# Optimization experiments

Hardware: AMD Instinct MI355X
Metric: run time of the kernel (lower is better)

Reference implementation:

```python
import jax, jax.numpy as jnp
import numpy as np
import math

B, C, LQ, LK = 8, 128, 2048, 2048

def setup_inputs() -> dict:
    key = jax.random.key(0)
    k1, k2, k3, k4 = jax.random.split(key, 4)
    return {
        "proj_query": jax.random.normal(k1, (B, C, LQ), dtype=jnp.float32),
        "proj_key": jax.random.normal(k2, (B, C, LK), dtype=jnp.float32),
        "proj_val": jax.random.normal(k3, (B, C, LK), dtype=jnp.float32),
        "padding_mask": jax.random.randint(k4, (B, LQ, LK), 0, 2, dtype=jnp.int32),
    }

def reference(proj_query, proj_key, proj_val, padding_mask):
    c = proj_query.shape[1]
    scale = 1.0 / math.sqrt(c)
    # energy: (B, Lq, Lk)
    energy = jnp.einsum('bcq,bck->bqk', proj_query, proj_key) * scale
    mask_f = padding_mask.astype(energy.dtype)
    attention = jax.nn.softmax(energy + jnp.log(mask_f + 1e-9), axis=-1)
    attention = attention * mask_f
    # out: (B, C, Lq)
    out = jnp.einsum('bck,bqk->bcq', proj_val, attention)
    return out, attention
```

## Files before the change

### kernel.cpp

```cpp
#include <hip/hip_runtime.h>
#include <hip/hip_bf16.h>
#include <math.h>

constexpr int NB  = 8;
constexpr int NC  = 128;
constexpr int NLQ = 2048;
constexpr int NLK = 2048;
#define SCALE 0.08838834764831845f

typedef _Float16 h8  __attribute__((ext_vector_type(8)));
typedef _Float16 h4v __attribute__((ext_vector_type(4)));
typedef float    f4  __attribute__((ext_vector_type(4)));
typedef int      i4  __attribute__((ext_vector_type(4)));

__global__ __launch_bounds__(256)
void trans_f32_h16(const float* __restrict__ in, _Float16* __restrict__ out)
{
    __shared__ float tile[32][33];
    const int b  = blockIdx.z;
    const int l0 = blockIdx.x * 32;
    const int c0 = blockIdx.y * 32;
    const int tx = threadIdx.x, ty = threadIdx.y;
    const float* ip = in + ((size_t)(b * NC + c0 + ty)) * NLK + l0 + tx;
    #pragma unroll
    for (int j = 0; j < 4; ++j)
        tile[ty + j * 8][tx] = ip[(size_t)j * 8 * NLK];
    __syncthreads();
    _Float16* op = out + ((size_t)(b * NLK + l0 + ty)) * NC + c0 + tx;
    #pragma unroll
    for (int j = 0; j < 4; ++j)
        op[(size_t)j * 8 * NC] = (_Float16)tile[tx][ty + j * 8];
}

__global__ __launch_bounds__(256)
void cvt_f32_h16(const float* __restrict__ in, _Float16* __restrict__ out, int n4)
{
    const int i = blockIdx.x * blockDim.x + threadIdx.x;
    if (i < n4) {
        const f4 v = *(const f4*)&in[(size_t)i * 4];
        h4v h;
        #pragma unroll
        for (int j = 0; j < 4; ++j) h[j] = (_Float16)v[j];
        *(h4v*)&out[(size_t)i * 4] = h;
    }
}

constexpr int KSTR = 136;
constexpr int PSTR = 72;

__global__ __launch_bounds__(512, 6)
void attn_main(const _Float16* __restrict__ Qt, const _Float16* __restrict__ Kt,
               const _Float16* __restrict__ Vh, const int* __restrict__ Mp,
               float* __restrict__ outP, float* __restrict__ attnP)
{
    __shared__ _Float16 Kl[2][64 * KSTR];
    __shared__ _Float16 pad[2][32 * PSTR];
    __shared__ float sred[32][4];

    const int tid  = threadIdx.x;
    const int w    = tid >> 6;
    const int lane = tid & 63;
    const int lo   = lane & 15;
    const int g    = lane >> 4;
    const int qsub = w & 1;
    const int kh   = w >> 1;

    const int bid   = blockIdx.x;
    const int b     = bid & 7;
    const int q0    = (bid >> 3) * 32;
    const int qbase = q0 + qsub * 16;

    const int krow = tid >> 3, kcs = (tid & 7) * 16;

    h8 aQ[4];
    {
        const _Float16* qr = &Qt[((size_t)(b * NLQ + qbase + lo)) * NC];
        #pragma unroll
        for (int cc = 0; cc < 4; ++cc) aQ[cc] = *(const h8*)&qr[cc * 32 + g * 8];
    }
    const int* mbase = &Mp[((size_t)(b * NLQ + qbase + lo)) * NLK + kh * 16 + g * 4];

    {
        const _Float16* s0 = &Kt[((size_t)(b * NLK + krow)) * NC + kcs];
        const h8 x = *(const h8*)s0, y = *(const h8*)(s0 + 8);
        _Float16* d0 = &Kl[0][krow * KSTR + kcs];
        *(h8*)d0 = x; *(h8*)(d0 + 8) = y;
    }
    i4 mm = *(const i4*)&mbase[0];
    __syncthreads();

    float os = 0.f;
    unsigned long long pk0 = 0ull, pk1 = 0ull;
    for (int t = 0; t < 32; ++t) {
        const int p = t & 1, tn = (t + 1 < 32) ? t + 1 : 31;
        const _Float16* ksp = &Kt[((size_t)(b * NLK + tn * 64 + krow)) * NC + kcs];
        const h8 nk0 = *(const h8*)ksp, nk1 = *(const h8*)(ksp + 8);
        const i4 mmn = *(const i4*)&mbase[(size_t)tn * 64];
        const unsigned int nib = (mm[0] & 1) | ((mm[1] & 1) << 1)
                               | ((mm[2] & 1) << 2) | ((mm[3] & 1) << 3);
        if (t < 16) pk0 |= (unsigned long long)nib << (t * 4);
        else        pk1 |= (unsigned long long)nib << ((t - 16) * 4);
        const _Float16* kr = &Kl[p][(kh * 16 + lo) * KSTR + g * 8];
        f4 d = {0.f, 0.f, 0.f, 0.f};
        d = __builtin_amdgcn_mfma_f32_16x16x32_f16(*(const h8*)&kr[0],  aQ[0], d, 0, 0, 0);
        d = __builtin_amdgcn_mfma_f32_16x16x32_f16(*(const h8*)&kr[32], aQ[1], d, 0, 0, 0);
        d = __builtin_amdgcn_mfma_f32_16x16x32_f16(*(const h8*)&kr[64], aQ[2], d, 0, 0, 0);
        d = __builtin_amdgcn_mfma_f32_16x16x32_f16(*(const h8*)&kr[96], aQ[3], d, 0, 0, 0);
        #pragma unroll
        for (int r = 0; r < 4; ++r)
            os += ((nib >> r) & 1u) ? __expf(d[r] * SCALE) : 0.f;
        _Float16* kd = &Kl[p ^ 1][krow * KSTR + kcs];
        *(h8*)kd = nk0; *(h8*)(kd + 8) = nk1;
        mm = mmn;
        __syncthreads();
    }
    os += __shfl_xor(os, 16);
    os += __shfl_xor(os, 32);
    if (lane < 16) sred[qsub * 16 + lane][kh] = os;
    __syncthreads();
    float inv;
    {
        const float S = sred[qsub * 16 + lo][0] + sred[qsub * 16 + lo][1]
                      + sred[qsub * 16 + lo][2] + sred[qsub * 16 + lo][3];
        inv = S > 0.f ? 1.0f / S : 0.f;
    }

    {
        const _Float16* s0 = &Kt[((size_t)(b * NLK + krow)) * NC + kcs];
        const h8 x = *(const h8*)s0, y = *(const h8*)(s0 + 8);
        _Float16* d0 = &Kl[0][krow * KSTR + kcs];
        *(h8*)d0 = x; *(h8*)(d0 + 8) = y;
    }
    const _Float16* vbase = &Vh[((size_t)(b * NC + w * 16 + lo)) * NLK + g * 8];
    h8 vn0 = *(const h8*)&vbase[0];
    h8 vn1 = *(const h8*)&vbase[32];
    __syncthreads();

    {
        const unsigned int nib = (unsigned int)(pk0 & 0xFull);
        const _Float16* kr = &Kl[0][(kh * 16 + lo) * KSTR + g * 8];
        f4 d = {0.f, 0.f, 0.f, 0.f};
        d = __builtin_amdgcn_mfma_f32_16x16x32_f16(*(const h8*)&kr[0],  aQ[0], d, 0, 0, 0);
        d = __builtin_amdgcn_mfma_f32_16x16x32_f16(*(const h8*)&kr[32], aQ[1], d, 0, 0, 0);
        d = __builtin_amdgcn_mfma_f32_16x16x32_f16(*(const h8*)&kr[64], aQ[2], d, 0, 0, 0);
        d = __builtin_amdgcn_mfma_f32_16x16x32_f16(*(const h8*)&kr[96], aQ[3], d, 0, 0, 0);
        h4v ph;
        #pragma unroll
        for (int r = 0; r < 4; ++r)
            ph[r] = ((nib >> r) & 1u) ? (_Float16)(__expf(d[r] * SCALE) * inv)
                                      : (_Float16)0.f;
        *(h4v*)&pad[0][(qsub * 16 + lo) * PSTR + kh * 16 + g * 4] = ph;
        const _Float16* ksp = &Kt[((size_t)(b * NLK + 64 + krow)) * NC + kcs];
        const h8 nk0 = *(const h8*)ksp, nk1 = *(const h8*)(ksp + 8);
        _Float16* kd = &Kl[1][krow * KSTR + kcs];
        *(h8*)kd = nk0; *(h8*)(kd + 8) = nk1;
    }

    f4 acc0 = {0.f, 0.f, 0.f, 0.f}, acc1 = {0.f, 0.f, 0.f, 0.f};
    const int arow = w * 4 + (lane >> 4);
    const int acol = (lane & 15) * 4;

    for (int t = 0; t < 32; ++t) {
        __syncthreads();
        const int bt = t & 1;
        const h8 v0 = vn0, v1 = vn1;
        if (t < 31) {
            const _Float16* vt = vbase + (size_t)(t + 1) * 64;
            vn0 = *(const h8*)&vt[0];
            vn1 = *(const h8*)&vt[32];
        }
        h8 kn0, kn1;
        if (t < 30) {
            const _Float16* ksp = &Kt[((size_t)(b * NLK + (t + 2) * 64 + krow)) * NC + kcs];
            kn0 = *(const h8*)ksp; kn1 = *(const h8*)(ksp + 8);
        }
        {
            const h4v ph = *(const h4v*)&pad[bt][arow * PSTR + acol];
            f4 av;
            #pragma unroll
            for (int i = 0; i < 4; ++i) av[i] = (float)ph[i];
            *(f4*)&attnP[((size_t)(b * NLQ + q0 + arow)) * NLK + t * 64 + acol] = av;
        }
        {
            const h8 pa00 = *(const h8*)&pad[bt][lo * PSTR + g * 8];
            const h8 pa01 = *(const h8*)&pad[bt][lo * PSTR + 32 + g * 8];
            const h8 pa10 = *(const h8*)&pad[bt][(16 + lo) * PSTR + g * 8];
            const h8 pa11 = *(const h8*)&pad[bt][(16 + lo) * PSTR + 32 + g * 8];
            acc0 = __builtin_amdgcn_mfma_f32_16x16x32_f16(pa00, v0, acc0, 0, 0, 0);
            acc0 = __builtin_amdgcn_mfma_f32_16x16x32_f16(pa01, v1, acc0, 0, 0, 0);
            acc1 = __builtin_amdgcn_mfma_f32_16x16x32_f16(pa10, v0, acc1, 0, 0, 0);
            acc1 = __builtin_amdgcn_mfma_f32_16x16x32_f16(pa11, v1, acc1, 0, 0, 0);
        }
        if (t < 31) {
            const int tt = t + 1;
            const unsigned long long sel = (tt & 16) ? pk1 : pk0;
            const unsigned int nib = (unsigned int)((sel >> ((tt & 15) * 4)) & 0xFull);
            const _Float16* kr = &Kl[tt & 1][(kh * 16 + lo) * KSTR + g * 8];
            f4 d = {0.f, 0.f, 0.f, 0.f};
            d = __builtin_amdgcn_mfma_f32_16x16x32_f16(*(const h8*)&kr[0],  aQ[0], d, 0, 0, 0);
            d = __builtin_amdgcn_mfma_f32_16x16x32_f16(*(const h8*)&kr[32], aQ[1], d, 0, 0, 0);
            d = __builtin_amdgcn_mfma_f32_16x16x32_f16(*(const h8*)&kr[64], aQ[2], d, 0, 0, 0);
            d = __builtin_amdgcn_mfma_f32_16x16x32_f16(*(const h8*)&kr[96], aQ[3], d, 0, 0, 0);
            h4v ph;
            #pragma unroll
            for (int r = 0; r < 4; ++r)
                ph[r] = ((nib >> r) & 1u) ? (_Float16)(__expf(d[r] * SCALE) * inv)
                                          : (_Float16)0.f;
            *(h4v*)&pad[bt ^ 1][(qsub * 16 + lo) * PSTR + kh * 16 + g * 4] = ph;
        }
        if (t < 30) {
            _Float16* kd = &Kl[bt][krow * KSTR + kcs];
            *(h8*)kd = kn0; *(h8*)(kd + 8) = kn1;
        }
    }
    *(f4*)&outP[((size_t)(b * NC + w * 16 + lo)) * NLQ + q0 + g * 4]      = acc0;
    *(f4*)&outP[((size_t)(b * NC + w * 16 + lo)) * NLQ + q0 + 16 + g * 4] = acc1;
}

constexpr int QT_F = 32;
constexpr int SPAD_F = 2056;

__global__ __launch_bounds__(512, 2)
void attn_fallback(const float* __restrict__ Qp, const float* __restrict__ Kp,
                   const float* __restrict__ Vp, const int* __restrict__ Mp,
                   float* __restrict__ outP, float* __restrict__ attnP)
{
    __shared__ _Float16 Sh[QT_F][SPAD_F];
    __shared__ float mred[4][QT_F];
    __shared__ float sred[4][QT_F];

    const int tid  = threadIdx.x;
    const int w    = tid >> 6;
    const int lane = tid & 63;
    const int lo   = lane & 15;
    const int g    = lane >> 4;
    const int qg   = w & 1;
    const int nh   = w >> 1;
    const int b    = blockIdx.y;
    const int q0   = blockIdx.x * QT_F;

    h8 aQ[4];
    {
        const int q = q0 + qg * 16 + lo;
        #pragma unroll
        for (int cc = 0; cc < 4; ++cc) {
            const float* qp = &Qp[((size_t)(b * NC + cc * 32 + g * 8)) * NLQ + q];
            #pragma unroll
            for (int j = 0; j < 8; ++j) aQ[cc][j] = (_Float16)qp[(size_t)j * NLQ];
        }
    }
    float mx[4] = {-INFINITY, -INFINITY, -INFINITY, -INFINITY};
    for (int t = 0; t < 32; ++t) {
        const int n0 = nh * 512 + t * 16;
        f4 d = {0.f, 0.f, 0.f, 0.f};
        #pragma unroll
        for (int cc = 0; cc < 4; ++cc) {
            const float* kp = &Kp[((size_t)(b * NC + cc * 32 + g * 8)) * NLK + n0 + lo];
            h8 bk;
            #pragma unroll
            for (int j = 0; j < 8; ++j) bk[j] = (_Float16)kp[(size_t)j * NLK];
            d = __builtin_amdgcn_mfma_f32_16x16x32_f16(aQ[cc], bk, d, 0, 0, 0);
        }
        const int* mp = &Mp[((size_t)(b * NLQ + q0 + qg * 16 + g * 4)) * NLK + n0 + lo];
        #pragma unroll
        for (int r = 0; r < 4; ++r) {
            float e = d[r] * SCALE;
            const int mv = mp[(size_t)r * NLK];
            e = mv ? e : -INFINITY;
            const _Float16 eh = (_Float16)e;
            mx[r] = fmaxf(mx[r], (float)eh);
            Sh[qg * 16 + g * 4 + r][n0 + lo] = eh;
        }
    }
    #pragma unroll
    for (int off = 1; off < 16; off <<= 1) {
        #pragma unroll
        for (int r = 0; r < 4; ++r) mx[r] = fmaxf(mx[r], __shfl_xor(mx[r], off));
    }
    if (lo == 0) {
        #pragma unroll
        for (int r = 0; r < 4; ++r) mred[nh][qg * 16 + g * 4 + r] = mx[r];
    }
    __syncthreads();
    for (int rr = 0; rr < 16; ++rr) {
        const int row = qg * 16 + rr;
        float m = fmaxf(fmaxf(mred[0][row], mred[1][row]), fmaxf(mred[2][row], mred[3][row]));
        if (m < -1e30f) m = 0.f;
        float s = 0.f;
        #pragma unroll
        for (int it = 0; it < 2; ++it) {
            const int kb = nh * 512 + it * 256 + lane * 4;
            h4v v = *(const h4v*)&Sh[row][kb];
            s += __expf((float)v[0] - m) + __expf((float)v[1] - m)
               + __expf((float)v[2] - m) + __expf((float)v[3] - m);
        }
        #pragma unroll
        for (int off = 1; off < 64; off <<= 1) s += __shfl_xor(s, off);
        if (lane == 0) sred[nh][row] = s;
    }
    __syncthreads();
    for (int rr = 0; rr < 16; ++rr) {
        const int row = qg * 16 + rr;
        float m = fmaxf(fmaxf(mred[0][row], mred[1][row]), fmaxf(mred[2][row], mred[3][row]));
        if (m < -1e30f) m = 0.f;
        const float s = sred[0][row] + sred[1][row] + sred[2][row] + sred[3][row];
        const float inv = s > 0.f ? 1.0f / s : 0.f;
        #pragma unroll
        for (int it = 0; it < 2; ++it) {
            const int kb = nh * 512 + it * 256 + lane * 4;
            h4v v = *(const h4v*)&Sh[row][kb];
            f4 a;
            #pragma unroll
            for (int i = 0; i < 4; ++i) a[i] = __expf((float)v[i] - m) * inv;
            *(f4*)&attnP[((size_t)(b * NLQ + q0 + row)) * NLK + kb] = a;
            h4v hv;
            #pragma unroll
            for (int i = 0; i < 4; ++i) hv[i] = (_Float16)a[i];
            *(h4v*)&Sh[row][kb] = hv;
        }
    }
    __syncthreads();
    f4 acc[2] = {{0.f,0.f,0.f,0.f},{0.f,0.f,0.f,0.f}};
    for (int kt = 0; kt < 64; ++kt) {
        const int k0 = kt * 32;
        const h8 a = *(const h8*)&Sh[qg * 16 + lo][k0 + g * 8];
        #pragma unroll
        for (int ct = 0; ct < 2; ++ct) {
            const int c = nh * 32 + ct * 16 + lo;
            const float* vp = &Vp[((size_t)(b * NC + c)) * NLK + k0 + g * 8];
            const f4 v0 = *(const f4*)vp;
            const f4 v1 = *(const f4*)(vp + 4);
            h8 bv;
            #pragma unroll
            for (int j = 0; j < 4; ++j) { bv[j] = (_Float16)v0[j]; bv[4 + j] = (_Float16)v1[j]; }
            acc[ct] = __builtin_amdgcn_mfma_f32_16x16x32_f16(a, bv, acc[ct], 0, 0, 0);
        }
    }
    #pragma unroll
    for (int ct = 0; ct < 2; ++ct) {
        const int c = nh * 32 + ct * 16 + lo;
        const int q = q0 + qg * 16 + g * 4;
        *(f4*)&outP[((size_t)(b * NC + c)) * NLQ + q] = acc[ct];
    }
}

extern "C" void kernel_launch(void* const* d_in, const int* in_sizes, int n_in,
                              void* d_out, int out_size, void* d_ws, size_t ws_size,
                              hipStream_t stream) {
    const float* Qp = (const float*)d_in[0];
    const float* Kp = (const float*)d_in[1];
    const float* Vp = (const float*)d_in[2];
    const int*   Mp = (const int*)d_in[3];
    float* outP  = (float*)d_out;
    float* attnP = outP + (size_t)NB * NC * NLQ;

    const size_t telem = (size_t)NB * NC * NLK;
    const size_t need  = 3 * telem * sizeof(_Float16);

    if (ws_size >= need) {
        _Float16* Qt = (_Float16*)d_ws;
        _Float16* Kt = Qt + telem;
        _Float16* Vh = Kt + telem;
        dim3 tb(32, 8);
        trans_f32_h16<<<dim3(NLQ / 32, NC / 32, NB), tb, 0, stream>>>(Qp, Qt);
        trans_f32_h16<<<dim3(NLK / 32, NC / 32, NB), tb, 0, stream>>>(Kp, Kt);
        cvt_f32_h16<<<(int)(telem / 4 + 255) / 256, 256, 0, stream>>>(Vp, Vh, (int)(telem / 4));
        attn_main<<<dim3(NB * (NLQ / 32)), dim3(512), 0, stream>>>(Qt, Kt, Vh, Mp, outP, attnP);
    } else {
        dim3 grid(NLQ / QT_F, NB);
        attn_fallback<<<grid, dim3(512), 0, stream>>>(Qp, Kp, Vp, Mp, outP, attnP);
    }
}
```

Measured before the change: 108.1 us.

## Use fixed-shift exponent and spill unnormalized probabilities to a global scratch buffer

Adds a new main kernel that skips online max tracking by applying a constant exponent shift, justified by bounded logits. It writes unnormalized fp16 probabilities for each 32x2048 query block to a global workspace. A second pass reads them back to emit normalized attention and to run the PV MFMA, with V streamed from global memory. This removes the rescaling and LDS staging of P, at the cost of an extra 64 MB scratch round-trip and the risk of overflow or underflow if the logits are not bounded. It runs only when the workspace is large enough.

```diff
diff --git a/kernel.cpp b/kernel.cpp
--- a/kernel.cpp
+++ b/kernel.cpp
@@ -7,6 +7,7 @@
 constexpr int NLQ = 2048;
 constexpr int NLK = 2048;
 #define SCALE 0.08838834764831845f
+#define EXPSH -8.317766166719343f
 
 typedef _Float16 h8  __attribute__((ext_vector_type(8)));
 typedef _Float16 h4v __attribute__((ext_vector_type(4)));
@@ -45,13 +46,151 @@
     }
 }
 
+__global__ __launch_bounds__(512, 4)
+void attn_main_ws(const _Float16* __restrict__ Qt, const _Float16* __restrict__ Kt,
+                  const _Float16* __restrict__ Vh, const int* __restrict__ Mp,
+                  _Float16* __restrict__ Pws,
+                  float* __restrict__ outP, float* __restrict__ attnP)
+{
+    __shared__ _Float16 Kl[2][8192];
+    __shared__ float sred[32][4];
+    __shared__ float invtab[32];
+
+    const int tid  = threadIdx.x;
+    const int w    = tid >> 6;
+    const int lane = tid & 63;
+    const int lo   = lane & 15;
+    const int g    = lane >> 4;
+    const int qsub = w & 1;
+    const int kh   = w >> 1;
+
+    const int bid   = blockIdx.x;
+    const int b     = bid & 7;
+    const int q0    = (bid >> 3) * 32;
+    const int qbase = q0 + qsub * 16;
+
+    _Float16* const Pb = Pws + (size_t)bid * 65536;
+
+    const int s1 = tid + 512;
+    const _Float16* src0 = &Kt[((size_t)(b * NLK + (tid >> 8) * 16 + (tid & 15))) * NC
+                               + ((tid >> 6) & 3) * 32 + ((tid >> 4) & 3) * 8];
+    const _Float16* src1 = &Kt[((size_t)(b * NLK + (s1 >> 8) * 16 + (s1 & 15))) * NC
+                               + ((s1 >> 6) & 3) * 32 + ((s1 >> 4) & 3) * 8];
+    const size_t kstep = (size_t)64 * NC;
+
+    h8 aQ[4];
+    {
+        const _Float16* qr = &Qt[((size_t)(b * NLQ + qbase + lo)) * NC];
+        #pragma unroll
+        for (int cc = 0; cc < 4; ++cc) aQ[cc] = *(const h8*)&qr[cc * 32 + g * 8];
+    }
+    const int* mbase = &Mp[((size_t)(b * NLQ + qbase + lo)) * NLK + kh * 16 + g * 4];
+    const int pwoff = (qsub * 2 + (kh >> 1)) * 512
+                    + (lo + 16 * ((kh & 1) * 2 + (g >> 1))) * 8 + (g & 1) * 4;
+
+    {
+        const h8 x0 = *(const h8*)src0, x1 = *(const h8*)src1;
+        *(h8*)&Kl[0][tid * 8] = x0;
+        *(h8*)&Kl[0][s1 * 8]  = x1;
+    }
+    i4 mm = *(const i4*)mbase;
+    __syncthreads();
+
+    float os = 0.f;
+    for (int t = 0; t < 32; ++t) {
+        h8 n0, n1; i4 mmn;
+        if (t < 31) {
+            n0 = *(const h8*)(src0 + (size_t)(t + 1) * kstep);
+            n1 = *(const h8*)(src1 + (size_t)(t + 1) * kstep);
+            mmn = *(const i4*)&mbase[(size_t)(t + 1) * 64];
+        }
+        const _Float16* kf = &Kl[t & 1][kh * 2048];
+        const h8 f0 = *(const h8*)&kf[0 * 512 + lane * 8];
+        const h8 f1 = *(const h8*)&kf[1 * 512 + lane * 8];
+        const h8 f2 = *(const h8*)&kf[2 * 512 + lane * 8];
+        const h8 f3 = *(const h8*)&kf[3 * 512 + lane * 8];
+        f4 d = {0.f, 0.f, 0.f, 0.f};
+        d = __builtin_amdgcn_mfma_f32_16x16x32_f16(f0, aQ[0], d, 0, 0, 0);
+        d = __builtin_amdgcn_mfma_f32_16x16x32_f16(f1, aQ[1], d, 0, 0, 0);
+        d = __builtin_amdgcn_mfma_f32_16x16x32_f16(f2, aQ[2], d, 0, 0, 0);
+        d = __builtin_amdgcn_mfma_f32_16x16x32_f16(f3, aQ[3], d, 0, 0, 0);
+        const unsigned int nib = (mm[0] & 1) | ((mm[1] & 1) << 1)
+                               | ((mm[2] & 1) << 2) | ((mm[3] & 1) << 3);
+        h4v ph;
+        #pragma unroll
+        for (int r = 0; r < 4; ++r) {
+            const float pv = ((nib >> r) & 1u) ? __expf(d[r] * SCALE + EXPSH) : 0.f;
+            ph[r] = (_Float16)pv;
+            os += pv;
+        }
+        *(h4v*)&Pb[(size_t)t * 2048 + pwoff] = ph;
+        if (t < 31) {
+            *(h8*)&Kl[(t + 1) & 1][tid * 8] = n0;
+            *(h8*)&Kl[(t + 1) & 1][s1 * 8]  = n1;
+            mm = mmn;
+        }
+        __syncthreads();
+    }
+    os += __shfl_xor(os, 16);
+    os += __shfl_xor(os, 32);
+    if (lane < 16) sred[qsub * 16 + lane][kh] = os;
+    __syncthreads();
+    if (tid < 32) {
+        const float S = sred[tid][0] + sred[tid][1] + sred[tid][2] + sred[tid][3];
+        invtab[tid] = S > 0.f ? 1.0f / S : 0.f;
+    }
+    __syncthreads();
+
+    const int arow = w * 4 + (lane >> 4);
+    const int k4   = (lane & 15) * 4;
+    const int soff = ((arow >> 4) * 2 + (k4 >> 5)) * 512
+                   + ((arow & 15) + 16 * ((k4 & 31) >> 3)) * 8 + (k4 & 7);
+    const float invA = invtab[arow];
+    float* const arp = &attnP[((size_t)(b * NLQ + q0 + arow)) * NLK + k4];
+
+    const _Float16* vb = &Vh[((size_t)(b * NC + w * 16 + lo)) * NLK + g * 8];
+    h8 vc0 = *(const h8*)&vb[0];
+    h8 vc1 = *(const h8*)&vb[32];
+
+    f4 acc0 = {0.f, 0.f, 0.f, 0.f}, acc1 = {0.f, 0.f, 0.f, 0.f};
+    for (int t = 0; t < 32; ++t) {
+        const _Float16* pb = Pb + (size_t)t * 2048;
+        const h8 pa00 = *(const h8*)&pb[0 * 512 + lane * 8];
+        const h8 pa01 = *(const h8*)&pb[1 * 512 + lane * 8];
+        const h8 pa10 = *(const h8*)&pb[2 * 512 + lane * 8];
+        const h8 pa11 = *(const h8*)&pb[3 * 512 + lane * 8];
+        const h4v ps  = *(const h4v*)&pb[soff];
+        const h8 v0 = vc0, v1 = vc1;
+        if (t < 31) {
+            const _Float16* vt = vb + (size_t)(t + 1) * 64;
+            vc0 = *(const h8*)&vt[0];
+            vc1 = *(const h8*)&vt[32];
+        }
+        f4 av;
+        #pragma unroll
+        for (int i = 0; i < 4; ++i) av[i] = (float)ps[i] * invA;
+        *(f4*)&arp[(size_t)t * 64] = av;
+        acc0 = __builtin_amdgcn_mfma_f32_16x16x32_f16(pa00, v0, acc0, 0, 0, 0);
+        acc0 = __builtin_amdgcn_mfma_f32_16x16x32_f16(pa01, v1, acc0, 0, 0, 0);
+        acc1 = __builtin_amdgcn_mfma_f32_16x16x32_f16(pa10, v0, acc1, 0, 0, 0);
+        acc1 = __builtin_amdgcn_mfma_f32_16x16x32_f16(pa11, v1, acc1, 0, 0, 0);
+    }
+    #pragma unroll
+    for (int r = 0; r < 4; ++r) {
+        acc0[r] *= invtab[g * 4 + r];
+        acc1[r] *= invtab[16 + g * 4 + r];
+    }
+    *(f4*)&outP[((size_t)(b * NC + w * 16 + lo)) * NLQ + q0 + g * 4]      = acc0;
+    *(f4*)&outP[((size_t)(b * NC + w * 16 + lo)) * NLQ + q0 + 16 + g * 4] = acc1;
+}
+
 constexpr int KSTR = 136;
 constexpr int PSTR = 72;
 
 __global__ __launch_bounds__(512, 6)
-void attn_main(const _Float16* __restrict__ Qt, const _Float16* __restrict__ Kt,
-               const _Float16* __restrict__ Vh, const int* __restrict__ Mp,
-               float* __restrict__ outP, float* __restrict__ attnP)
+void attn_main_small(const _Float16* __restrict__ Qt, const _Float16* __restrict__ Kt,
+                     const _Float16* __restrict__ Vh, const int* __restrict__ Mp,
+                     float* __restrict__ outP, float* __restrict__ attnP)
 {
     __shared__ _Float16 Kl[2][64 * KSTR];
     __shared__ _Float16 pad[2][32 * PSTR];
@@ -355,9 +494,11 @@
     float* attnP = outP + (size_t)NB * NC * NLQ;
 
     const size_t telem = (size_t)NB * NC * NLK;
-    const size_t need  = 3 * telem * sizeof(_Float16);
-
-    if (ws_size >= need) {
+    const size_t need0 = 3 * telem * sizeof(_Float16);
+    const size_t pbytes = (size_t)512 * 65536 * sizeof(_Float16);
+    const size_t need1 = need0 + pbytes;
+
+    if (ws_size >= need0) {
         _Float16* Qt = (_Float16*)d_ws;
         _Float16* Kt = Qt + telem;
         _Float16* Vh = Kt + telem;
@@ -365,7 +506,12 @@
         trans_f32_h16<<<dim3(NLQ / 32, NC / 32, NB), tb, 0, stream>>>(Qp, Qt);
         trans_f32_h16<<<dim3(NLK / 32, NC / 32, NB), tb, 0, stream>>>(Kp, Kt);
         cvt_f32_h16<<<(int)(telem / 4 + 255) / 256, 256, 0, stream>>>(Vp, Vh, (int)(telem / 4));
-        attn_main<<<dim3(NB * (NLQ / 32)), dim3(512), 0, stream>>>(Qt, Kt, Vh, Mp, outP, attnP);
+        if (ws_size >= need1) {
+            _Float16* Pws = Vh + telem;
+            attn_main_ws<<<dim3(NB * (NLQ / 32)), dim3(512), 0, stream>>>(Qt, Kt, Vh, Mp, Pws, outP, attnP);
+        } else {
+            attn_main_small<<<dim3(NB * (NLQ / 32)), dim3(512), 0, stream>>>(Qt, Kt, Vh, Mp, outP, attnP);
+        }
     } else {
         dim3 grid(NLQ / QT_F, NB);
         attn_fallback<<<grid, dim3(512), 0, stream>>>(Qp, Kp, Vp, Mp, outP, attnP);
```

Result: slower. 145.9 us (+34.9%).

## Triple-buffer K tiles with two-ahead prefetch and swizzle P layout

Applied to the files above, without the earlier changes.

Replaces the double-buffered K shared-memory tiles with three rotating buffers, so global loads run two iterations ahead and the LDS store of the next tile happens before the barrier. The P tile moves to a fragment-ordered layout, so MFMA operand reads become contiguous per lane, and the K row stride changes to 140. This aims to hide global load latency and cut LDS bank conflicts. In exchange it uses more shared memory and registers, and the occupancy hint drops from 6 to 4 blocks per CU.

```diff
diff --git a/kernel.cpp b/kernel.cpp
--- a/kernel.cpp
+++ b/kernel.cpp
@@ -45,16 +45,17 @@
     }
 }
 
-constexpr int KSTR = 136;
-constexpr int PSTR = 72;
-
-__global__ __launch_bounds__(512, 6)
+constexpr int KSTR = 140;
+
+__global__ __launch_bounds__(512, 4)
 void attn_main(const _Float16* __restrict__ Qt, const _Float16* __restrict__ Kt,
                const _Float16* __restrict__ Vh, const int* __restrict__ Mp,
                float* __restrict__ outP, float* __restrict__ attnP)
 {
-    __shared__ _Float16 Kl[2][64 * KSTR];
-    __shared__ _Float16 pad[2][32 * PSTR];
+    __shared__ _Float16 Kl0[64 * KSTR];
+    __shared__ _Float16 Kl1[64 * KSTR];
+    __shared__ _Float16 Kl2[64 * KSTR];
+    __shared__ _Float16 pad[2][2048];
     __shared__ float sred[32][4];
 
     const int tid  = threadIdx.x;
@@ -79,28 +80,43 @@
         for (int cc = 0; cc < 4; ++cc) aQ[cc] = *(const h8*)&qr[cc * 32 + g * 8];
     }
     const int* mbase = &Mp[((size_t)(b * NLQ + qbase + lo)) * NLK + kh * 16 + g * 4];
-
-    {
-        const _Float16* s0 = &Kt[((size_t)(b * NLK + krow)) * NC + kcs];
-        const h8 x = *(const h8*)s0, y = *(const h8*)(s0 + 8);
-        _Float16* d0 = &Kl[0][krow * KSTR + kcs];
+    const _Float16* kstage = &Kt[((size_t)(b * NLK + krow)) * NC + kcs];
+    const size_t kstep = (size_t)64 * NC;
+    const int fro = (kh * 16 + lo) * KSTR + g * 8;
+
+    {
+        const h8 x = *(const h8*)kstage, y = *(const h8*)(kstage + 8);
+        _Float16* d0 = &Kl0[krow * KSTR + kcs];
         *(h8*)d0 = x; *(h8*)(d0 + 8) = y;
     }
-    i4 mm = *(const i4*)&mbase[0];
-    __syncthreads();
-
+    h8 kH0, kH1;
+    {
+        const _Float16* s1p = kstage + kstep;
+        kH0 = *(const h8*)s1p; kH1 = *(const h8*)(s1p + 8);
+    }
+    i4 mA = *(const i4*)&mbase[0];
+    i4 mB = *(const i4*)&mbase[64];
+    __syncthreads();
+
+    _Float16 *bufA = Kl0, *bufB = Kl1, *bufC = Kl2;
     float os = 0.f;
     unsigned long long pk0 = 0ull, pk1 = 0ull;
     for (int t = 0; t < 32; ++t) {
-        const int p = t & 1, tn = (t + 1 < 32) ? t + 1 : 31;
-        const _Float16* ksp = &Kt[((size_t)(b * NLK + tn * 64 + krow)) * NC + kcs];
-        const h8 nk0 = *(const h8*)ksp, nk1 = *(const h8*)(ksp + 8);
-        const i4 mmn = *(const i4*)&mbase[(size_t)tn * 64];
-        const unsigned int nib = (mm[0] & 1) | ((mm[1] & 1) << 1)
-                               | ((mm[2] & 1) << 2) | ((mm[3] & 1) << 3);
+        h8 kF0 = kH0, kF1 = kH1; i4 mC = mB;
+        if (t + 2 < 32) {
+            const _Float16* ksp = kstage + (size_t)(t + 2) * kstep;
+            kF0 = *(const h8*)ksp; kF1 = *(const h8*)(ksp + 8);
+            mC = *(const i4*)&mbase[(size_t)(t + 2) * 64];
+        }
+        if (t + 1 < 32) {
+            _Float16* kd = &bufB[krow * KSTR + kcs];
+            *(h8*)kd = kH0; *(h8*)(kd + 8) = kH1;
+        }
+        const unsigned int nib = (mA[0] & 1) | ((mA[1] & 1) << 1)
+                               | ((mA[2] & 1) << 2) | ((mA[3] & 1) << 3);
         if (t < 16) pk0 |= (unsigned long long)nib << (t * 4);
         else        pk1 |= (unsigned long long)nib << ((t - 16) * 4);
-        const _Float16* kr = &Kl[p][(kh * 16 + lo) * KSTR + g * 8];
+        const _Float16* kr = &bufA[fro];
         f4 d = {0.f, 0.f, 0.f, 0.f};
         d = __builtin_amdgcn_mfma_f32_16x16x32_f16(*(const h8*)&kr[0],  aQ[0], d, 0, 0, 0);
         d = __builtin_amdgcn_mfma_f32_16x16x32_f16(*(const h8*)&kr[32], aQ[1], d, 0, 0, 0);
@@ -109,10 +125,9 @@
         #pragma unroll
         for (int r = 0; r < 4; ++r)
             os += ((nib >> r) & 1u) ? __expf(d[r] * SCALE) : 0.f;
-        _Float16* kd = &Kl[p ^ 1][krow * KSTR + kcs];
-        *(h8*)kd = nk0; *(h8*)(kd + 8) = nk1;
-        mm = mmn;
         __syncthreads();
+        kH0 = kF0; kH1 = kF1; mA = mB; mB = mC;
+        _Float16* tmp = bufA; bufA = bufB; bufB = bufC; bufC = tmp;
     }
     os += __shfl_xor(os, 16);
     os += __shfl_xor(os, 32);
@@ -125,20 +140,30 @@
         inv = S > 0.f ? 1.0f / S : 0.f;
     }
 
-    {
-        const _Float16* s0 = &Kt[((size_t)(b * NLK + krow)) * NC + kcs];
-        const h8 x = *(const h8*)s0, y = *(const h8*)(s0 + 8);
-        _Float16* d0 = &Kl[0][krow * KSTR + kcs];
+    const int pwoff = (qsub * 2 + (kh >> 1)) * 512
+                    + (lo + 16 * ((kh & 1) * 2 + (g >> 1))) * 8 + (g & 1) * 4;
+    const int arow = w * 4 + (lane >> 4);
+    const int k4   = (lane & 15) * 4;
+    const int soff = ((arow >> 4) * 2 + (k4 >> 5)) * 512
+                   + ((arow & 15) + 16 * ((k4 & 31) >> 3)) * 8 + (k4 & 7);
+    float* const arp = &attnP[((size_t)(b * NLQ + q0 + arow)) * NLK + k4];
+
+    {
+        const h8 x = *(const h8*)kstage, y = *(const h8*)(kstage + 8);
+        _Float16* d0 = &Kl0[krow * KSTR + kcs];
         *(h8*)d0 = x; *(h8*)(d0 + 8) = y;
-    }
-    const _Float16* vbase = &Vh[((size_t)(b * NC + w * 16 + lo)) * NLK + g * 8];
-    h8 vn0 = *(const h8*)&vbase[0];
-    h8 vn1 = *(const h8*)&vbase[32];
-    __syncthreads();
-
+        const _Float16* s1p = kstage + kstep;
+        kH0 = *(const h8*)s1p; kH1 = *(const h8*)(s1p + 8);
+    }
+    const _Float16* vb = &Vh[((size_t)(b * NC + w * 16 + lo)) * NLK + g * 8];
+    h8 vA0 = *(const h8*)&vb[0];
+    h8 vA1 = *(const h8*)&vb[32];
+    __syncthreads();
+
+    bufA = Kl0; bufB = Kl1; bufC = Kl2;
     {
         const unsigned int nib = (unsigned int)(pk0 & 0xFull);
-        const _Float16* kr = &Kl[0][(kh * 16 + lo) * KSTR + g * 8];
+        const _Float16* kr = &bufA[fro];
         f4 d = {0.f, 0.f, 0.f, 0.f};
         d = __builtin_amdgcn_mfma_f32_16x16x32_f16(*(const h8*)&kr[0],  aQ[0], d, 0, 0, 0);
         d = __builtin_amdgcn_mfma_f32_16x16x32_f16(*(const h8*)&kr[32], aQ[1], d, 0, 0, 0);
@@ -149,53 +174,48 @@
         for (int r = 0; r < 4; ++r)
             ph[r] = ((nib >> r) & 1u) ? (_Float16)(__expf(d[r] * SCALE) * inv)
                                       : (_Float16)0.f;
-        *(h4v*)&pad[0][(qsub * 16 + lo) * PSTR + kh * 16 + g * 4] = ph;
-        const _Float16* ksp = &Kt[((size_t)(b * NLK + 64 + krow)) * NC + kcs];
-        const h8 nk0 = *(const h8*)ksp, nk1 = *(const h8*)(ksp + 8);
-        _Float16* kd = &Kl[1][krow * KSTR + kcs];
-        *(h8*)kd = nk0; *(h8*)(kd + 8) = nk1;
+        *(h4v*)&pad[0][pwoff] = ph;
     }
 
     f4 acc0 = {0.f, 0.f, 0.f, 0.f}, acc1 = {0.f, 0.f, 0.f, 0.f};
-    const int arow = w * 4 + (lane >> 4);
-    const int acol = (lane & 15) * 4;
-
     for (int t = 0; t < 32; ++t) {
+        h8 kF0 = kH0, kF1 = kH1, vF0 = vA0, vF1 = vA1;
+        if (t + 2 < 32) {
+            const _Float16* ksp = kstage + (size_t)(t + 2) * kstep;
+            kF0 = *(const h8*)ksp; kF1 = *(const h8*)(ksp + 8);
+        }
+        if (t + 1 < 32) {
+            const _Float16* vt = vb + (size_t)(t + 1) * 64;
+            vF0 = *(const h8*)&vt[0];
+            vF1 = *(const h8*)&vt[32];
+        }
+        if (t + 1 < 32) {
+            _Float16* kd = &bufB[krow * KSTR + kcs];
+            *(h8*)kd = kH0; *(h8*)(kd + 8) = kH1;
+        }
         __syncthreads();
-        const int bt = t & 1;
-        const h8 v0 = vn0, v1 = vn1;
-        if (t < 31) {
-            const _Float16* vt = vbase + (size_t)(t + 1) * 64;
-            vn0 = *(const h8*)&vt[0];
-            vn1 = *(const h8*)&vt[32];
-        }
-        h8 kn0, kn1;
-        if (t < 30) {
-            const _Float16* ksp = &Kt[((size_t)(b * NLK + (t + 2) * 64 + krow)) * NC + kcs];
-            kn0 = *(const h8*)ksp; kn1 = *(const h8*)(ksp + 8);
-        }
         {
-            const h4v ph = *(const h4v*)&pad[bt][arow * PSTR + acol];
+            const h4v ps = *(const h4v*)&pad[t & 1][soff];
             f4 av;
             #pragma unroll
-            for (int i = 0; i < 4; ++i) av[i] = (float)ph[i];
-            *(f4*)&attnP[((size_t)(b * NLQ + q0 + arow)) * NLK + t * 64 + acol] = av;
+            for (int i = 0; i < 4; ++i) av[i] = (float)ps[i];
+            *(f4*)&arp[(size_t)t * 64] = av;
         }
         {
-            const h8 pa00 = *(const h8*)&pad[bt][lo * PSTR + g * 8];
-            const h8 pa01 = *(const h8*)&pad[bt][lo * PSTR + 32 + g * 8];
-            const h8 pa10 = *(const h8*)&pad[bt][(16 + lo) * PSTR + g * 8];
-            const h8 pa11 = *(const h8*)&pad[bt][(16 + lo) * PSTR + 32 + g * 8];
-            acc0 = __builtin_amdgcn_mfma_f32_16x16x32_f16(pa00, v0, acc0, 0, 0, 0);
-            acc0 = __builtin_amdgcn_mfma_f32_16x16x32_f16(pa01, v1, acc0, 0, 0, 0);
-            acc1 = __builtin_amdgcn_mfma_f32_16x16x32_f16(pa10, v0, acc1, 0, 0, 0);
-            acc1 = __builtin_amdgcn_mfma_f32_16x16x32_f16(pa11, v1, acc1, 0, 0, 0);
-        }
-        if (t < 31) {
+            const h8 pa00 = *(const h8*)&pad[t & 1][0 * 512 + lane * 8];
+            const h8 pa01 = *(const h8*)&pad[t & 1][1 * 512 + lane * 8];
+            const h8 pa10 = *(const h8*)&pad[t & 1][2 * 512 + lane * 8];
+            const h8 pa11 = *(const h8*)&pad[t & 1][3 * 512 + lane * 8];
+            acc0 = __builtin_amdgcn_mfma_f32_16x16x32_f16(pa00, vA0, acc0, 0, 0, 0);
+            acc0 = __builtin_amdgcn_mfma_f32_16x16x32_f16(pa01, vA1, acc0, 0, 0, 0);
+            acc1 = __builtin_amdgcn_mfma_f32_16x16x32_f16(pa10, vA0, acc1, 0, 0, 0);
+            acc1 = __builtin_amdgcn_mfma_f32_16x16x32_f16(pa11, vA1, acc1, 0, 0, 0);
+        }
+        if (t + 1 < 32) {
             const int tt = t + 1;
             const unsigned long long sel = (tt & 16) ? pk1 : pk0;
             const unsigned int nib = (unsigned int)((sel >> ((tt & 15) * 4)) & 0xFull);
-            const _Float16* kr = &Kl[tt & 1][(kh * 16 + lo) * KSTR + g * 8];
+            const _Float16* kr = &bufB[fro];
             f4 d = {0.f, 0.f, 0.f, 0.f};
             d = __builtin_amdgcn_mfma_f32_16x16x32_f16(*(const h8*)&kr[0],  aQ[0], d, 0, 0, 0);
             d = __builtin_amdgcn_mfma_f32_16x16x32_f16(*(const h8*)&kr[32], aQ[1], d, 0, 0, 0);
@@ -206,12 +226,10 @@
             for (int r = 0; r < 4; ++r)
                 ph[r] = ((nib >> r) & 1u) ? (_Float16)(__expf(d[r] * SCALE) * inv)
                                           : (_Float16)0.f;
-            *(h4v*)&pad[bt ^ 1][(qsub * 16 + lo) * PSTR + kh * 16 + g * 4] = ph;
-        }
-        if (t < 30) {
-            _Float16* kd = &Kl[bt][krow * KSTR + kcs];
-            *(h8*)kd = kn0; *(h8*)(kd + 8) = kn1;
-        }
+            *(h4v*)&pad[(t + 1) & 1][pwoff] = ph;
+        }
+        kH0 = kF0; kH1 = kF1; vA0 = vF0; vA1 = vF1;
+        _Float16* tmp = bufA; bufA = bufB; bufB = bufC; bufC = tmp;
     }
     *(f4*)&outP[((size_t)(b * NC + w * 16 + lo)) * NLQ + q0 + g * 4]      = acc0;
     *(f4*)&outP[((size_t)(b * NC + w * 16 + lo)) * NLQ + q0 + 16 + g * 4] = acc1;
```

Measured after the change: 184.2 us. 1.7x slower.
